# Optimization experiments

Measured on AMD Instinct MI355X. Metric: run time of the kernel, lower is better.

The kernel has to match this reference:

```python
import jax, jax.numpy as jnp
import numpy as np

N, D, H, G = 4096, 256, 4, 16
HEAD_DIM = D // H
LN_EPS = 1e-5
TEMP = 5.0


def setup_inputs() -> dict:
    key = jax.random.key(0)
    ks = jax.random.split(key, 12)
    s = 0.05  # weight init scale
    nrm = lambda k, shp: jax.random.normal(k, shp, jnp.float32) * s
    return {
        "x": jax.random.normal(ks[0], (N, D), jnp.float32),
        "Wq": nrm(ks[1], (D, D)), "bq": jnp.zeros((D,), jnp.float32),
        "Wk": nrm(ks[2], (D, D)), "bk": jnp.zeros((D,), jnp.float32),
        "Wv": nrm(ks[3], (D, D)), "bv": jnp.zeros((D,), jnp.float32),
        "Wv1": nrm(ks[4], (D, D // 2)), "bv1": jnp.zeros((D // 2,), jnp.float32),
        "Wv2": nrm(ks[5], (D // 2, 1)), "bv2": jnp.zeros((1,), jnp.float32),
        "Wc1": nrm(ks[6], (2 * D, D)), "bc1": jnp.zeros((D,), jnp.float32),
        "Wc2": nrm(ks[7], (D, 1)), "bc2": jnp.zeros((1,), jnp.float32),
        "gamma": jnp.ones((D,), jnp.float32),
        "beta": jnp.zeros((D,), jnp.float32),
        "batch": jnp.sort(jax.random.randint(ks[8], (N,), 0, G)),
    }


def reference(x, Wq, bq, Wk, bk, Wv, bv, Wv1, bv1, Wv2, bv2,
              Wc1, bc1, Wc2, bc2, gamma, beta, batch):
    n = x.shape[0]
    # multi-head projections -> [N, H, head_dim]
    Q = (x @ Wq + bq).reshape(n, H, HEAD_DIM)
    K = (x @ Wk + bk).reshape(n, H, HEAD_DIM)
    V = (x @ Wv + bv).reshape(n, H, HEAD_DIM)

    # dense scores [N, N, H], block-diagonal mask by graph membership
    scores = jnp.einsum('nhd,mhd->nmh', Q, K) / np.sqrt(HEAD_DIM).astype(np.float32)
    same_graph = (batch[:, None] == batch[None, :])  # [N, N]
    scores = jnp.where(same_graph[:, :, None], scores, -jnp.inf)
    probs = jax.nn.softmax(scores, axis=1)  # softmax over keys m (dim=1, as in torch)
    # dropout is identity in eval mode
    attended = jnp.einsum('nmh,mhd->nhd', probs, V).reshape(n, D)

    # vulnerability detector MLP: D -> D/2 -> 1, sigmoid
    vuln = jax.nn.sigmoid(jax.nn.relu(x @ Wv1 + bv1) @ Wv2 + bv2)[:, 0]

    # global max pool per graph, broadcast back to nodes
    graph_ctx = jax.ops.segment_max(x, batch, num_segments=G, indices_are_sorted=True)[batch]
    combined = jnp.concatenate([x, graph_ctx], axis=1)  # [N, 2D]
    ctx = jax.nn.sigmoid(jnp.tanh(combined @ Wc1 + bc1) @ Wc2 + bc2)[:, 0]

    mha_avg = probs.mean(axis=(1, 2))  # [N]
    w = 0.6 * vuln + 0.3 * ctx + 0.1 * mha_avg

    # per-graph segment softmax with temperature 5.0
    w5 = w * TEMP
    seg_max = jax.ops.segment_max(w5, batch, num_segments=G, indices_are_sorted=True)[batch]
    e = jnp.exp(w5 - seg_max)
    seg_sum = jax.ops.segment_sum(e, batch, num_segments=G, indices_are_sorted=True)[batch]
    att = e / seg_sum  # [N]

    out = attended * att[:, None] + x  # residual
    # LayerNorm over last dim
    mu = out.mean(axis=-1, keepdims=True)
    var = out.var(axis=-1, keepdims=True)
    out = (out - mu) * jax.lax.rsqrt(var + LN_EPS) * gamma + beta
    return out, att
```

## Files before the change

kernel.cpp:

```cpp
#include <hip/hip_runtime.h>
#include <math.h>

#define N_NODES 4096
#define DIM 256
#define NH 4
#define NG 16
#define LN_EPS 1e-5f
#define TEMP 5.0f
#define RSLACK 4160
#define PS_STRIDE 72
#define BS_STRIDE 264
#define QT_MAX 24
#define KC3 3
#define ATTN_BLOCKS (NG * QT_MAX * KC3)

typedef __attribute__((ext_vector_type(8))) short short8;
typedef __attribute__((ext_vector_type(4))) short short4_t;
typedef __attribute__((ext_vector_type(4))) float f32x4;

__device__ __forceinline__ unsigned short f2bf(float f) {
    unsigned u = __builtin_bit_cast(unsigned, f);
    u += 0x7FFFu + ((u >> 16) & 1u);
    return (unsigned short)(u >> 16);
}
__device__ __forceinline__ float bf2f(unsigned short u) {
    return __builtin_bit_cast(float, (unsigned)u << 16);
}
__device__ __forceinline__ float fsigmoid(float z) { return 1.f / (1.f + __expf(-z)); }
__device__ __forceinline__ float ftanh(float z) {
    float t = __expf(2.f * z);
    return (t - 1.f) / (t + 1.f);
}
__device__ __forceinline__ int seg_search(const int* __restrict__ batch, int g) {
    int lo = 0, hi = N_NODES;
    while (lo < hi) {
        int mid = (lo + hi) >> 1;
        if (batch[mid] < g) lo = mid + 1; else hi = mid;
    }
    return lo;
}

__device__ __forceinline__ short8 afrag_f32(const float* __restrict__ x, int row, int k0) {
    float4 a = *(const float4*)&x[(size_t)row * 256 + k0];
    float4 b = *(const float4*)&x[(size_t)row * 256 + k0 + 4];
    short8 r = {(short)f2bf(a.x), (short)f2bf(a.y), (short)f2bf(a.z), (short)f2bf(a.w),
                (short)f2bf(b.x), (short)f2bf(b.y), (short)f2bf(b.z), (short)f2bf(b.w)};
    return r;
}

__device__ __forceinline__ void ldsB(const float* __restrict__ W, int ws, int bn,
                                     unsigned short* __restrict__ Bs) {
    int c4 = (threadIdx.x & 15) * 4;
    int r0 = threadIdx.x >> 4;
    for (int p = 0; p < 16; ++p) {
        int k = p * 16 + r0;
        float4 wv = *(const float4*)&W[(size_t)k * ws + bn + c4];
        Bs[(c4 + 0) * BS_STRIDE + k] = f2bf(wv.x);
        Bs[(c4 + 1) * BS_STRIDE + k] = f2bf(wv.y);
        Bs[(c4 + 2) * BS_STRIDE + k] = f2bf(wv.z);
        Bs[(c4 + 3) * BS_STRIDE + k] = f2bf(wv.w);
    }
    __syncthreads();
}

__global__ __launch_bounds__(256) void k1_kernel(
    const float* __restrict__ x,
    const float* __restrict__ Wq, const float* __restrict__ bq,
    const float* __restrict__ Wk, const float* __restrict__ bk,
    const float* __restrict__ Wv, const float* __restrict__ bv,
    const float* __restrict__ Wv1, const float* __restrict__ bv1,
    const float* __restrict__ Wv2, const float* __restrict__ Wc1,
    const float* __restrict__ bc1, const int* __restrict__ batch,
    unsigned short* __restrict__ Qb, unsigned short* __restrict__ Kb,
    unsigned short* __restrict__ Vt, float* __restrict__ vacc2,
    float* __restrict__ Tpre, float* __restrict__ gcw, int* __restrict__ seg) {
    __shared__ __align__(16) char smem[64 * BS_STRIDE * 2];
    int id = blockIdx.x, tid = threadIdx.x;
    if (id < 16) {
        int g = id;
        int s = seg_search(batch, g), e = seg_search(batch, g + 1);
        float* red = (float*)smem;
        float* gl  = (float*)smem + 1024;
        int c4 = (tid & 63) * 4, way = tid >> 6;
        float4 mx = {-INFINITY, -INFINITY, -INFINITY, -INFINITY};
        for (int i = s + way; i < e; i += 4) {
            float4 v = *(const float4*)&x[(size_t)i * DIM + c4];
            mx.x = fmaxf(mx.x, v.x); mx.y = fmaxf(mx.y, v.y);
            mx.z = fmaxf(mx.z, v.z); mx.w = fmaxf(mx.w, v.w);
        }
        *(float4*)&red[way * 256 + c4] = mx;
        __syncthreads();
        if (way == 0) {
#pragma unroll
            for (int j = 0; j < 4; ++j) {
                float mm = fmaxf(fmaxf(red[c4 + j], red[256 + c4 + j]),
                                 fmaxf(red[512 + c4 + j], red[768 + c4 + j]));
                gl[c4 + j] = bf2f(f2bf(mm));
            }
        }
        __syncthreads();
        float a0 = 0.f, a1 = 0.f, a2 = 0.f, a3 = 0.f;
        for (int k = 0; k < 256; k += 4) {
            a0 += gl[k + 0] * Wc1[(size_t)(256 + k + 0) * 256 + tid];
            a1 += gl[k + 1] * Wc1[(size_t)(256 + k + 1) * 256 + tid];
            a2 += gl[k + 2] * Wc1[(size_t)(256 + k + 2) * 256 + tid];
            a3 += gl[k + 3] * Wc1[(size_t)(256 + k + 3) * 256 + tid];
        }
        gcw[g * 256 + tid] = (a0 + a1) + (a2 + a3);
        return;
    }
    if (id == 16) {
        if (tid <= NG) seg[tid] = seg_search(batch, tid);
        return;
    }
    int u = id - 17;
    unsigned short* Bs = (unsigned short*)smem;
    int w = tid >> 6, lane = tid & 63, m = lane & 15, quad = lane >> 4;
    if (u < 768) {
        int z = u >> 8, r = u & 255, bx = r & 63, by = r >> 6;
        const float* W = (z == 0) ? Wq : (z == 1) ? Wk : Wv;
        const float* bias = (z == 0) ? bq : (z == 1) ? bk : bv;
        ldsB(W, 256, by * 64, Bs);
        int rowA = bx * 64 + 16 * w + m;
        short8 a[8];
#pragma unroll
        for (int ks = 0; ks < 8; ++ks) a[ks] = afrag_f32(x, rowA, ks * 32 + quad * 8);
        int node0 = bx * 64 + 16 * w + quad * 4;
#pragma unroll
        for (int nt = 0; nt < 4; ++nt) {
            f32x4 acc = {0.f, 0.f, 0.f, 0.f};
#pragma unroll
            for (int ks = 0; ks < 8; ++ks) {
                short8 b = *(const short8*)&Bs[(nt * 16 + m) * BS_STRIDE + ks * 32 + quad * 8];
                acc = __builtin_amdgcn_mfma_f32_16x16x32_bf16(a[ks], b, acc, 0, 0, 0);
            }
            int col = by * 64 + nt * 16 + m;
            float bb = bias[col];
            if (z == 0) {
#pragma unroll
                for (int r2 = 0; r2 < 4; ++r2)
                    Qb[(size_t)(node0 + r2) * 256 + col] = f2bf((acc[r2] + bb) * 0.125f);
            } else if (z == 1) {
#pragma unroll
                for (int r2 = 0; r2 < 4; ++r2)
                    Kb[(size_t)(node0 + r2) * 256 + col] = f2bf(acc[r2] + bb);
            } else {
                short4_t pk = {(short)f2bf(acc[0] + bb), (short)f2bf(acc[1] + bb),
                               (short)f2bf(acc[2] + bb), (short)f2bf(acc[3] + bb)};
                *(short4_t*)&Vt[(size_t)col * RSLACK + node0] = pk;
            }
        }
    } else if (u < 896) {
        int r = u - 768, bx = r & 63, by = r >> 6;
        ldsB(Wv1, 128, by * 64, Bs);
        int rowA = bx * 64 + 16 * w + m;
        short8 a[8];
#pragma unroll
        for (int ks = 0; ks < 8; ++ks) a[ks] = afrag_f32(x, rowA, ks * 32 + quad * 8);
        int node0 = bx * 64 + 16 * w + quad * 4;
        float psum[4] = {0.f, 0.f, 0.f, 0.f};
#pragma unroll
        for (int nt = 0; nt < 4; ++nt) {
            f32x4 acc = {0.f, 0.f, 0.f, 0.f};
#pragma unroll
            for (int ks = 0; ks < 8; ++ks) {
                short8 b = *(const short8*)&Bs[(nt * 16 + m) * BS_STRIDE + ks * 32 + quad * 8];
                acc = __builtin_amdgcn_mfma_f32_16x16x32_bf16(a[ks], b, acc, 0, 0, 0);
            }
            int col = by * 64 + nt * 16 + m;
            float bb = bv1[col], wv = Wv2[col];
#pragma unroll
            for (int r2 = 0; r2 < 4; ++r2) psum[r2] += fmaxf(acc[r2] + bb, 0.f) * wv;
        }
#pragma unroll
        for (int r2 = 0; r2 < 4; ++r2) {
#pragma unroll
            for (int mm = 1; mm < 16; mm <<= 1) psum[r2] += __shfl_xor(psum[r2], mm);
            if (m == 0) vacc2[(size_t)(node0 + r2) * 2 + by] = psum[r2];
        }
    } else {
        int r = u - 896, bx = r & 63, by = r >> 6;
        ldsB(Wc1, 256, by * 64, Bs);
        int rowA = bx * 64 + 16 * w + m;
        short8 a[8];
#pragma unroll
        for (int ks = 0; ks < 8; ++ks) a[ks] = afrag_f32(x, rowA, ks * 32 + quad * 8);
        int node0 = bx * 64 + 16 * w + quad * 4;
#pragma unroll
        for (int nt = 0; nt < 4; ++nt) {
            f32x4 acc = {0.f, 0.f, 0.f, 0.f};
#pragma unroll
            for (int ks = 0; ks < 8; ++ks) {
                short8 b = *(const short8*)&Bs[(nt * 16 + m) * BS_STRIDE + ks * 32 + quad * 8];
                acc = __builtin_amdgcn_mfma_f32_16x16x32_bf16(a[ks], b, acc, 0, 0, 0);
            }
            int col = by * 64 + nt * 16 + m;
            float bb = bc1[col];
#pragma unroll
            for (int r2 = 0; r2 < 4; ++r2)
                Tpre[(size_t)(node0 + r2) * 256 + col] = acc[r2] + bb;
        }
    }
}

__global__ __launch_bounds__(256) void k2_kernel(
    const float* __restrict__ Tpre, const float* __restrict__ gcw,
    const float* __restrict__ Wc2, const int* __restrict__ batch,
    const unsigned short* __restrict__ Qb, const unsigned short* __restrict__ Kb,
    const unsigned short* __restrict__ Vt, const int* __restrict__ seg,
    unsigned short* __restrict__ Opart, float* __restrict__ Lpart,
    float* __restrict__ cacc) {
    __shared__ __align__(16) unsigned short Ps[4 * 16 * PS_STRIDE];
    int tid = threadIdx.x;
    if (blockIdx.x < 256) {
        int nl = tid >> 4, cs = (tid & 15) * 16;
        int node = blockIdx.x * 16 + nl;
        int g = batch[node];
        float sum = 0.f;
#pragma unroll
        for (int j = 0; j < 16; ++j) {
            int c = cs + j;
            sum += ftanh(Tpre[(size_t)node * 256 + c] + gcw[g * 256 + c]) * Wc2[c];
        }
#pragma unroll
        for (int mm = 1; mm < 16; mm <<= 1) sum += __shfl_xor(sum, mm);
        if ((tid & 15) == 0) cacc[node] = sum;
        return;
    }
    int w = tid >> 6, lane = tid & 63, m = lane & 15, quad = lane >> 4;
    int wid = (blockIdx.x - 256) * 4 + w;
    int g = wid / (KC3 * QT_MAX * NH);
    int r1 = wid - g * (KC3 * QT_MAX * NH);
    int kc = r1 / (QT_MAX * NH);
    int r2i = r1 - kc * (QT_MAX * NH);
    int qt = r2i >> 2, h = r2i & 3;
    int s = seg[g], e = seg[g + 1];
    int q0 = s + qt * 16;
    int kst = s + kc * 128;
    if (q0 >= e || kst >= e) return;
    int ken = min(e, kst + 128);

    short8 qa0 = *(const short8*)&Qb[(size_t)(q0 + m) * 256 + h * 64 + quad * 8];
    short8 qa1 = *(const short8*)&Qb[(size_t)(q0 + m) * 256 + h * 64 + 32 + quad * 8];
    short8 ones = {16256, 16256, 16256, 16256, 16256, 16256, 16256, 16256};
    f32x4 O[4];
    f32x4 Lacc = {0.f, 0.f, 0.f, 0.f};
#pragma unroll
    for (int nt = 0; nt < 4; ++nt) O[nt] = (f32x4){0.f, 0.f, 0.f, 0.f};
    int wbase = w * 16 * PS_STRIDE;

    for (int k0 = kst; k0 < ken; k0 += 64) {
        f32x4 S[4];
#pragma unroll
        for (int nt = 0; nt < 4; ++nt) {
            int key = k0 + nt * 16 + m;
            short8 kb0 = *(const short8*)&Kb[(size_t)key * 256 + h * 64 + quad * 8];
            short8 kb1 = *(const short8*)&Kb[(size_t)key * 256 + h * 64 + 32 + quad * 8];
            f32x4 sa = {0.f, 0.f, 0.f, 0.f};
            sa = __builtin_amdgcn_mfma_f32_16x16x32_bf16(qa0, kb0, sa, 0, 0, 0);
            sa = __builtin_amdgcn_mfma_f32_16x16x32_bf16(qa1, kb1, sa, 0, 0, 0);
            S[nt] = sa;
        }
        __builtin_amdgcn_wave_barrier();
#pragma unroll
        for (int nt = 0; nt < 4; ++nt) {
            bool valid = (k0 + nt * 16 + m) < e;
#pragma unroll
            for (int r3 = 0; r3 < 4; ++r3) {
                float p = valid ? __expf(S[nt][r3]) : 0.f;
                Ps[wbase + (quad * 4 + r3) * PS_STRIDE + nt * 16 + m] = f2bf(p);
            }
        }
        __builtin_amdgcn_wave_barrier();
        short8 pa0 = *(const short8*)&Ps[wbase + m * PS_STRIDE + quad * 8];
        short8 pa1 = *(const short8*)&Ps[wbase + m * PS_STRIDE + 32 + quad * 8];
        Lacc = __builtin_amdgcn_mfma_f32_16x16x32_bf16(pa0, ones, Lacc, 0, 0, 0);
        Lacc = __builtin_amdgcn_mfma_f32_16x16x32_bf16(pa1, ones, Lacc, 0, 0, 0);
#pragma unroll
        for (int nt = 0; nt < 4; ++nt) {
            const unsigned short* vrow = &Vt[(size_t)(h * 64 + nt * 16 + m) * RSLACK + k0];
            short8 vb0 = *(const short8*)&vrow[quad * 8];
            short8 vb1 = *(const short8*)&vrow[32 + quad * 8];
            O[nt] = __builtin_amdgcn_mfma_f32_16x16x32_bf16(pa0, vb0, O[nt], 0, 0, 0);
            O[nt] = __builtin_amdgcn_mfma_f32_16x16x32_bf16(pa1, vb1, O[nt], 0, 0, 0);
        }
    }
#pragma unroll
    for (int r3 = 0; r3 < 4; ++r3) {
        int q = q0 + quad * 4 + r3;
        if (q < e) {
            if (m == 0) Lpart[((size_t)kc * N_NODES + q) * 4 + h] = Lacc[r3];
#pragma unroll
            for (int nt = 0; nt < 4; ++nt)
                Opart[((size_t)kc * N_NODES + q) * 256 + h * 64 + nt * 16 + m] =
                    f2bf(O[nt][r3]);
        }
    }
}

__global__ __launch_bounds__(256) void k3_kernel(
    const unsigned short* __restrict__ Opart, const float* __restrict__ Lpart,
    const float* __restrict__ x, const float* __restrict__ vacc2,
    const float* __restrict__ cacc, const float* __restrict__ bv2,
    const float* __restrict__ bc2, const float* __restrict__ gamma,
    const float* __restrict__ beta, const int* __restrict__ batch,
    const int* __restrict__ seg, float* __restrict__ out,
    float* __restrict__ att_out) {
    __shared__ float wsc[776];
    __shared__ float gm[8], gsum[8];
    __shared__ float r1[4], r2[4];
    int tid = threadIdx.x;
    int n0 = blockIdx.x * 8;
    int gf = batch[n0], gl = batch[n0 + 7];
    int s0 = seg[gf], e1 = seg[gl + 1];
    float vb = bv2[0], cb = bc2[0];
    for (int j = s0 + tid; j < e1; j += 256) {
        float2 vv = *(const float2*)&vacc2[(size_t)j * 2];
        wsc[j - s0] = TEMP * (0.6f * fsigmoid(vv.x + vv.y + vb) +
                              0.3f * fsigmoid(cacc[j] + cb) + 0.1f / 4096.f);
    }
    __syncthreads();
    for (int g = gf; g <= gl; ++g) {
        int gs_ = seg[g], ge = seg[g + 1];
        float mx = -1e30f;
        for (int j = gs_ + tid; j < ge; j += 256) mx = fmaxf(mx, wsc[j - s0]);
#pragma unroll
        for (int k2 = 32; k2; k2 >>= 1) mx = fmaxf(mx, __shfl_xor(mx, k2));
        if ((tid & 63) == 0) r1[tid >> 6] = mx;
        __syncthreads();
        mx = fmaxf(fmaxf(r1[0], r1[1]), fmaxf(r1[2], r1[3]));
        float sm = 0.f;
        for (int j = gs_ + tid; j < ge; j += 256) sm += __expf(wsc[j - s0] - mx);
#pragma unroll
        for (int k2 = 32; k2; k2 >>= 1) sm += __shfl_xor(sm, k2);
        __syncthreads();
        if ((tid & 63) == 0) r2[tid >> 6] = sm;
        __syncthreads();
        if (tid == 0) {
            gm[g - gf] = mx;
            gsum[g - gf] = r2[0] + r2[1] + r2[2] + r2[3];
        }
        __syncthreads();
    }
    int h = tid >> 6;
    for (int i = 0; i < 8; ++i) {
        int n = n0 + i;
        int g = batch[n];
        int s = seg[g], e = seg[g + 1];
        float att_n = __expf(wsc[n - s0] - gm[g - gf]) / gsum[g - gf];
        if (tid == 0) att_out[n] = att_n;
        float L = 0.f, O = 0.f;
#pragma unroll
        for (int c = 0; c < KC3; ++c) {
            bool valid = (s + c * 128) < e;
            float lv = Lpart[((size_t)c * N_NODES + n) * 4 + h];
            float ov = bf2f(Opart[((size_t)c * N_NODES + n) * 256 + tid]);
            if (valid) { L += lv; O += ov; }
        }
        float o = (O / L) * att_n + x[(size_t)n * 256 + tid];
        float s1 = o, s2 = o * o;
#pragma unroll
        for (int k2 = 32; k2; k2 >>= 1) {
            s1 += __shfl_xor(s1, k2);
            s2 += __shfl_xor(s2, k2);
        }
        __syncthreads();
        if ((tid & 63) == 0) { r1[tid >> 6] = s1; r2[tid >> 6] = s2; }
        __syncthreads();
        float mu = (r1[0] + r1[1] + r1[2] + r1[3]) * (1.f / 256.f);
        float ms = (r2[0] + r2[1] + r2[2] + r2[3]) * (1.f / 256.f);
        float rs = rsqrtf(ms - mu * mu + LN_EPS);
        out[(size_t)n * 256 + tid] = (o - mu) * rs * gamma[tid] + beta[tid];
    }
}

extern "C" void kernel_launch(void* const* d_in, const int* in_sizes, int n_in,
                              void* d_out, int out_size, void* d_ws, size_t ws_size,
                              hipStream_t stream) {
    const float* x     = (const float*)d_in[0];
    const float* Wq    = (const float*)d_in[1];
    const float* bq    = (const float*)d_in[2];
    const float* Wk    = (const float*)d_in[3];
    const float* bk    = (const float*)d_in[4];
    const float* Wv    = (const float*)d_in[5];
    const float* bv    = (const float*)d_in[6];
    const float* Wv1   = (const float*)d_in[7];
    const float* bv1   = (const float*)d_in[8];
    const float* Wv2   = (const float*)d_in[9];
    const float* bv2   = (const float*)d_in[10];
    const float* Wc1   = (const float*)d_in[11];
    const float* bc1   = (const float*)d_in[12];
    const float* Wc2   = (const float*)d_in[13];
    const float* bc2   = (const float*)d_in[14];
    const float* gamma = (const float*)d_in[15];
    const float* beta  = (const float*)d_in[16];
    const int*   batch = (const int*)d_in[17];

    float* out = (float*)d_out;
    float* att = out + N_NODES * DIM;

    float* vacc2 = (float*)d_ws;
    float* cacc  = vacc2 + N_NODES * 2;
    float* gcw   = cacc + N_NODES;
    float* Lpart = gcw + NG * DIM;
    float* Tpre  = Lpart + KC3 * N_NODES * 4;
    int*   seg   = (int*)(Tpre + N_NODES * DIM);
    unsigned short* Qb    = (unsigned short*)(seg + 32);
    unsigned short* Kb    = Qb + RSLACK * DIM;
    unsigned short* Vt    = Kb + RSLACK * DIM;
    unsigned short* Opart = Vt + DIM * RSLACK;

    k1_kernel<<<1169, 256, 0, stream>>>(x, Wq, bq, Wk, bk, Wv, bv, Wv1, bv1, Wv2,
                                        Wc1, bc1, batch, Qb, Kb, Vt, vacc2, Tpre,
                                        gcw, seg);
    k2_kernel<<<256 + ATTN_BLOCKS, 256, 0, stream>>>(Tpre, gcw, Wc2, batch,
                                                     Qb, Kb, Vt, seg,
                                                     Opart, Lpart, cacc);
    k3_kernel<<<N_NODES / 8, 256, 0, stream>>>(Opart, Lpart, x, vacc2, cacc,
                                               bv2, bc2, gamma, beta, batch, seg,
                                               out, att);
}
```

Measured before the change: 169.0 us.

## Pre-convert x and weights to bf16 once; fuse ctx tanh epilogue into GEMM

Adds a prep kernel that converts x to bf16 and transposes and converts the Q/K/V/Wv1/Wc1 weights to bf16 once. It also computes the per-graph max-pool context and zeroes the ctx accumulator. The GEMM kernel then loads bf16 tiles directly, so it no longer re-converts fp32 in each of its many blocks. The Wc1 GEMM now applies tanh, the graph context and Wc2 in its epilogue and atomically accumulates ctx, which removes the Tpre round trip and the separate ctx pass in k2. The cost is an extra kernel launch and floating-point atomics, which make the ctx sum order nondeterministic.

```diff
diff --git a/kernel.cpp b/kernel.cpp
--- a/kernel.cpp
+++ b/kernel.cpp
@@ -40,47 +40,22 @@
     return lo;
 }
 
-__device__ __forceinline__ short8 afrag_f32(const float* __restrict__ x, int row, int k0) {
-    float4 a = *(const float4*)&x[(size_t)row * 256 + k0];
-    float4 b = *(const float4*)&x[(size_t)row * 256 + k0 + 4];
-    short8 r = {(short)f2bf(a.x), (short)f2bf(a.y), (short)f2bf(a.z), (short)f2bf(a.w),
-                (short)f2bf(b.x), (short)f2bf(b.y), (short)f2bf(b.z), (short)f2bf(b.w)};
-    return r;
-}
-
-__device__ __forceinline__ void ldsB(const float* __restrict__ W, int ws, int bn,
-                                     unsigned short* __restrict__ Bs) {
-    int c4 = (threadIdx.x & 15) * 4;
-    int r0 = threadIdx.x >> 4;
-    for (int p = 0; p < 16; ++p) {
-        int k = p * 16 + r0;
-        float4 wv = *(const float4*)&W[(size_t)k * ws + bn + c4];
-        Bs[(c4 + 0) * BS_STRIDE + k] = f2bf(wv.x);
-        Bs[(c4 + 1) * BS_STRIDE + k] = f2bf(wv.y);
-        Bs[(c4 + 2) * BS_STRIDE + k] = f2bf(wv.z);
-        Bs[(c4 + 3) * BS_STRIDE + k] = f2bf(wv.w);
-    }
-    __syncthreads();
-}
-
-__global__ __launch_bounds__(256) void k1_kernel(
-    const float* __restrict__ x,
-    const float* __restrict__ Wq, const float* __restrict__ bq,
-    const float* __restrict__ Wk, const float* __restrict__ bk,
-    const float* __restrict__ Wv, const float* __restrict__ bv,
-    const float* __restrict__ Wv1, const float* __restrict__ bv1,
-    const float* __restrict__ Wv2, const float* __restrict__ Wc1,
-    const float* __restrict__ bc1, const int* __restrict__ batch,
-    unsigned short* __restrict__ Qb, unsigned short* __restrict__ Kb,
-    unsigned short* __restrict__ Vt, float* __restrict__ vacc2,
-    float* __restrict__ Tpre, float* __restrict__ gcw, int* __restrict__ seg) {
-    __shared__ __align__(16) char smem[64 * BS_STRIDE * 2];
+__global__ __launch_bounds__(256) void k0_kernel(
+    const float* __restrict__ x, const float* __restrict__ Wq,
+    const float* __restrict__ Wk, const float* __restrict__ Wv,
+    const float* __restrict__ Wv1, const float* __restrict__ Wc1,
+    const int* __restrict__ batch,
+    unsigned short* __restrict__ xb, unsigned short* __restrict__ WqT,
+    unsigned short* __restrict__ WkT, unsigned short* __restrict__ WvT,
+    unsigned short* __restrict__ Wv1T, unsigned short* __restrict__ Wc1aT,
+    float* __restrict__ gcw, int* __restrict__ seg, float* __restrict__ cacc) {
+    __shared__ float sred[1280];
     int id = blockIdx.x, tid = threadIdx.x;
     if (id < 16) {
         int g = id;
         int s = seg_search(batch, g), e = seg_search(batch, g + 1);
-        float* red = (float*)smem;
-        float* gl  = (float*)smem + 1024;
+        float* red = sred;
+        float* gl  = sred + 1024;
         int c4 = (tid & 63) * 4, way = tid >> 6;
         float4 mx = {-INFINITY, -INFINITY, -INFINITY, -INFINITY};
         for (int i = s + way; i < e; i += 4) {
@@ -111,20 +86,81 @@
     }
     if (id == 16) {
         if (tid <= NG) seg[tid] = seg_search(batch, tid);
+        for (int i = tid; i < N_NODES; i += 256) cacc[i] = 0.f;
         return;
     }
-    int u = id - 17;
-    unsigned short* Bs = (unsigned short*)smem;
+    if (id < 81) {
+        int row = (id - 17) * 64 + (tid >> 2);
+        int c0 = (tid & 3) * 64;
+        const float* src = &x[(size_t)row * 256 + c0];
+        unsigned short* dst = &xb[(size_t)row * 256 + c0];
+#pragma unroll
+        for (int j = 0; j < 8; ++j) {
+            float4 a = *(const float4*)&src[j * 8];
+            float4 b = *(const float4*)&src[j * 8 + 4];
+            short8 r = {(short)f2bf(a.x), (short)f2bf(a.y), (short)f2bf(a.z), (short)f2bf(a.w),
+                        (short)f2bf(b.x), (short)f2bf(b.y), (short)f2bf(b.z), (short)f2bf(b.w)};
+            *(short8*)&dst[j * 8] = r;
+        }
+        return;
+    }
+    int t = id - 81;
+    const float* W; unsigned short* WT; int ncols, tt;
+    if (t < 16)      { W = Wq;  WT = WqT;   ncols = 256; tt = t; }
+    else if (t < 32) { W = Wk;  WT = WkT;   ncols = 256; tt = t - 16; }
+    else if (t < 48) { W = Wv;  WT = WvT;   ncols = 256; tt = t - 32; }
+    else if (t < 64) { W = Wc1; WT = Wc1aT; ncols = 256; tt = t - 48; }
+    else             { W = Wv1; WT = Wv1T;  ncols = 128; tt = t - 64; }
+    int c0 = (ncols == 256) ? (tt & 3) * 64 : (tt & 1) * 64;
+    int k0 = (ncols == 256) ? (tt >> 2) * 64 : (tt >> 1) * 64;
+    int col = c0 + (tid >> 2);
+    int kk0 = k0 + (tid & 3) * 16;
+    short8 r0v, r1v;
+#pragma unroll
+    for (int kk = 0; kk < 8; ++kk)
+        r0v[kk] = (short)f2bf(W[(size_t)(kk0 + kk) * ncols + col]);
+#pragma unroll
+    for (int kk = 0; kk < 8; ++kk)
+        r1v[kk] = (short)f2bf(W[(size_t)(kk0 + 8 + kk) * ncols + col]);
+    *(short8*)&WT[(size_t)col * 256 + kk0] = r0v;
+    *(short8*)&WT[(size_t)col * 256 + kk0 + 8] = r1v;
+}
+
+__device__ __forceinline__ void ldsB_bf(const unsigned short* __restrict__ WT, int bn,
+                                        unsigned short* __restrict__ Bs) {
+    const short8* src = (const short8*)&WT[(size_t)bn * 256 + threadIdx.x * 64];
+    unsigned short* dst = &Bs[(threadIdx.x >> 2) * BS_STRIDE + (threadIdx.x & 3) * 64];
+#pragma unroll
+    for (int j = 0; j < 8; ++j) *(short8*)&dst[j * 8] = src[j];
+    __syncthreads();
+}
+
+__global__ __launch_bounds__(256) void k1_kernel(
+    const unsigned short* __restrict__ xb,
+    const unsigned short* __restrict__ WqT, const unsigned short* __restrict__ WkT,
+    const unsigned short* __restrict__ WvT, const unsigned short* __restrict__ Wv1T,
+    const unsigned short* __restrict__ Wc1aT,
+    const float* __restrict__ bq, const float* __restrict__ bk,
+    const float* __restrict__ bv, const float* __restrict__ bv1,
+    const float* __restrict__ Wv2, const float* __restrict__ bc1,
+    const float* __restrict__ Wc2, const float* __restrict__ gcw,
+    const int* __restrict__ batch,
+    unsigned short* __restrict__ Qb, unsigned short* __restrict__ Kb,
+    unsigned short* __restrict__ Vt, float* __restrict__ vacc2,
+    float* __restrict__ cacc) {
+    __shared__ __align__(16) unsigned short Bs[64 * BS_STRIDE];
+    int u = blockIdx.x, tid = threadIdx.x;
     int w = tid >> 6, lane = tid & 63, m = lane & 15, quad = lane >> 4;
     if (u < 768) {
         int z = u >> 8, r = u & 255, bx = r & 63, by = r >> 6;
-        const float* W = (z == 0) ? Wq : (z == 1) ? Wk : Wv;
+        const unsigned short* WT = (z == 0) ? WqT : (z == 1) ? WkT : WvT;
         const float* bias = (z == 0) ? bq : (z == 1) ? bk : bv;
-        ldsB(W, 256, by * 64, Bs);
+        ldsB_bf(WT, by * 64, Bs);
         int rowA = bx * 64 + 16 * w + m;
         short8 a[8];
 #pragma unroll
-        for (int ks = 0; ks < 8; ++ks) a[ks] = afrag_f32(x, rowA, ks * 32 + quad * 8);
+        for (int ks = 0; ks < 8; ++ks)
+            a[ks] = *(const short8*)&xb[(size_t)rowA * 256 + ks * 32 + quad * 8];
         int node0 = bx * 64 + 16 * w + quad * 4;
 #pragma unroll
         for (int nt = 0; nt < 4; ++nt) {
@@ -152,11 +188,12 @@
         }
     } else if (u < 896) {
         int r = u - 768, bx = r & 63, by = r >> 6;
-        ldsB(Wv1, 128, by * 64, Bs);
+        ldsB_bf(Wv1T, by * 64, Bs);
         int rowA = bx * 64 + 16 * w + m;
         short8 a[8];
 #pragma unroll
-        for (int ks = 0; ks < 8; ++ks) a[ks] = afrag_f32(x, rowA, ks * 32 + quad * 8);
+        for (int ks = 0; ks < 8; ++ks)
+            a[ks] = *(const short8*)&xb[(size_t)rowA * 256 + ks * 32 + quad * 8];
         int node0 = bx * 64 + 16 * w + quad * 4;
         float psum[4] = {0.f, 0.f, 0.f, 0.f};
 #pragma unroll
@@ -180,12 +217,16 @@
         }
     } else {
         int r = u - 896, bx = r & 63, by = r >> 6;
-        ldsB(Wc1, 256, by * 64, Bs);
+        ldsB_bf(Wc1aT, by * 64, Bs);
         int rowA = bx * 64 + 16 * w + m;
         short8 a[8];
 #pragma unroll
-        for (int ks = 0; ks < 8; ++ks) a[ks] = afrag_f32(x, rowA, ks * 32 + quad * 8);
+        for (int ks = 0; ks < 8; ++ks)
+            a[ks] = *(const short8*)&xb[(size_t)rowA * 256 + ks * 32 + quad * 8];
         int node0 = bx * 64 + 16 * w + quad * 4;
+        int g0 = batch[node0], g1 = batch[node0 + 1];
+        int g2 = batch[node0 + 2], g3 = batch[node0 + 3];
+        float psum[4] = {0.f, 0.f, 0.f, 0.f};
 #pragma unroll
         for (int nt = 0; nt < 4; ++nt) {
             f32x4 acc = {0.f, 0.f, 0.f, 0.f};
@@ -195,40 +236,30 @@
                 acc = __builtin_amdgcn_mfma_f32_16x16x32_bf16(a[ks], b, acc, 0, 0, 0);
             }
             int col = by * 64 + nt * 16 + m;
-            float bb = bc1[col];
-#pragma unroll
-            for (int r2 = 0; r2 < 4; ++r2)
-                Tpre[(size_t)(node0 + r2) * 256 + col] = acc[r2] + bb;
+            float bb = bc1[col], wc = Wc2[col];
+            const float* gc = &gcw[col];
+            psum[0] += ftanh(acc[0] + bb + gc[g0 * 256]) * wc;
+            psum[1] += ftanh(acc[1] + bb + gc[g1 * 256]) * wc;
+            psum[2] += ftanh(acc[2] + bb + gc[g2 * 256]) * wc;
+            psum[3] += ftanh(acc[3] + bb + gc[g3 * 256]) * wc;
+        }
+#pragma unroll
+        for (int r2 = 0; r2 < 4; ++r2) {
+#pragma unroll
+            for (int mm = 1; mm < 16; mm <<= 1) psum[r2] += __shfl_xor(psum[r2], mm);
+            if (m == 0) atomicAdd(&cacc[node0 + r2], psum[r2]);
         }
     }
 }
 
 __global__ __launch_bounds__(256) void k2_kernel(
-    const float* __restrict__ Tpre, const float* __restrict__ gcw,
-    const float* __restrict__ Wc2, const int* __restrict__ batch,
     const unsigned short* __restrict__ Qb, const unsigned short* __restrict__ Kb,
     const unsigned short* __restrict__ Vt, const int* __restrict__ seg,
-    unsigned short* __restrict__ Opart, float* __restrict__ Lpart,
-    float* __restrict__ cacc) {
+    unsigned short* __restrict__ Opart, float* __restrict__ Lpart) {
     __shared__ __align__(16) unsigned short Ps[4 * 16 * PS_STRIDE];
     int tid = threadIdx.x;
-    if (blockIdx.x < 256) {
-        int nl = tid >> 4, cs = (tid & 15) * 16;
-        int node = blockIdx.x * 16 + nl;
-        int g = batch[node];
-        float sum = 0.f;
-#pragma unroll
-        for (int j = 0; j < 16; ++j) {
-            int c = cs + j;
-            sum += ftanh(Tpre[(size_t)node * 256 + c] + gcw[g * 256 + c]) * Wc2[c];
-        }
-#pragma unroll
-        for (int mm = 1; mm < 16; mm <<= 1) sum += __shfl_xor(sum, mm);
-        if ((tid & 15) == 0) cacc[node] = sum;
-        return;
-    }
     int w = tid >> 6, lane = tid & 63, m = lane & 15, quad = lane >> 4;
-    int wid = (blockIdx.x - 256) * 4 + w;
+    int wid = blockIdx.x * 4 + w;
     int g = wid / (KC3 * QT_MAX * NH);
     int r1 = wid - g * (KC3 * QT_MAX * NH);
     int kc = r1 / (QT_MAX * NH);
@@ -403,19 +434,25 @@
     float* cacc  = vacc2 + N_NODES * 2;
     float* gcw   = cacc + N_NODES;
     float* Lpart = gcw + NG * DIM;
-    float* Tpre  = Lpart + KC3 * N_NODES * 4;
-    int*   seg   = (int*)(Tpre + N_NODES * DIM);
-    unsigned short* Qb    = (unsigned short*)(seg + 32);
+    int*   seg   = (int*)(Lpart + KC3 * N_NODES * 4);
+    unsigned short* xb    = (unsigned short*)(seg + 32);
+    unsigned short* WqT   = xb + N_NODES * DIM;
+    unsigned short* WkT   = WqT + DIM * DIM;
+    unsigned short* WvT   = WkT + DIM * DIM;
+    unsigned short* Wc1aT = WvT + DIM * DIM;
+    unsigned short* Wv1T  = Wc1aT + DIM * DIM;
+    unsigned short* Qb    = Wv1T + (DIM / 2) * DIM;
     unsigned short* Kb    = Qb + RSLACK * DIM;
     unsigned short* Vt    = Kb + RSLACK * DIM;
     unsigned short* Opart = Vt + DIM * RSLACK;
 
-    k1_kernel<<<1169, 256, 0, stream>>>(x, Wq, bq, Wk, bk, Wv, bv, Wv1, bv1, Wv2,
-                                        Wc1, bc1, batch, Qb, Kb, Vt, vacc2, Tpre,
-                                        gcw, seg);
-    k2_kernel<<<256 + ATTN_BLOCKS, 256, 0, stream>>>(Tpre, gcw, Wc2, batch,
-                                                     Qb, Kb, Vt, seg,
-                                                     Opart, Lpart, cacc);
+    k0_kernel<<<153, 256, 0, stream>>>(x, Wq, Wk, Wv, Wv1, Wc1, batch,
+                                       xb, WqT, WkT, WvT, Wv1T, Wc1aT,
+                                       gcw, seg, cacc);
+    k1_kernel<<<1152, 256, 0, stream>>>(xb, WqT, WkT, WvT, Wv1T, Wc1aT,
+                                        bq, bk, bv, bv1, Wv2, bc1, Wc2, gcw, batch,
+                                        Qb, Kb, Vt, vacc2, cacc);
+    k2_kernel<<<ATTN_BLOCKS, 256, 0, stream>>>(Qb, Kb, Vt, seg, Opart, Lpart);
     k3_kernel<<<N_NODES / 8, 256, 0, stream>>>(Opart, Lpart, x, vacc2, cacc,
                                                bv2, bc2, gamma, beta, batch, seg,
                                                out, att);
```

Measured after the change: 175.1 us. 3.6% more time.

## Drop key-chunk split in attention, prefetch V fragments, unroll gcw loads

Applied to the files above, without the earlier changes.

Each attention wave now covers the whole key range of its graph instead of one of three 128-key chunks. This removes the partial-result writes and the three-way merge in the final kernel, and the attention blocks are ordered before the context-MLP blocks. V fragments are loaded right after the QK MFMAs, ahead of the softmax, to hide load latency. The graph-context GEMV batches 32 weight loads per step, and the segment max loop is unrolled. The cost is fewer waves with longer serial loops, which lowers parallelism for large graphs.

```diff
diff --git a/kernel.cpp b/kernel.cpp
--- a/kernel.cpp
+++ b/kernel.cpp
@@ -11,8 +11,7 @@
 #define PS_STRIDE 72
 #define BS_STRIDE 264
 #define QT_MAX 24
-#define KC3 3
-#define ATTN_BLOCKS (NG * QT_MAX * KC3)
+#define K2_ATTN_BLOCKS (NG * QT_MAX)
 
 typedef __attribute__((ext_vector_type(8))) short short8;
 typedef __attribute__((ext_vector_type(4))) short short4_t;
@@ -83,6 +82,7 @@
         float* gl  = (float*)smem + 1024;
         int c4 = (tid & 63) * 4, way = tid >> 6;
         float4 mx = {-INFINITY, -INFINITY, -INFINITY, -INFINITY};
+#pragma unroll 8
         for (int i = s + way; i < e; i += 4) {
             float4 v = *(const float4*)&x[(size_t)i * DIM + c4];
             mx.x = fmaxf(mx.x, v.x); mx.y = fmaxf(mx.y, v.y);
@@ -99,14 +99,16 @@
             }
         }
         __syncthreads();
-        float a0 = 0.f, a1 = 0.f, a2 = 0.f, a3 = 0.f;
-        for (int k = 0; k < 256; k += 4) {
-            a0 += gl[k + 0] * Wc1[(size_t)(256 + k + 0) * 256 + tid];
-            a1 += gl[k + 1] * Wc1[(size_t)(256 + k + 1) * 256 + tid];
-            a2 += gl[k + 2] * Wc1[(size_t)(256 + k + 2) * 256 + tid];
-            a3 += gl[k + 3] * Wc1[(size_t)(256 + k + 3) * 256 + tid];
-        }
-        gcw[g * 256 + tid] = (a0 + a1) + (a2 + a3);
+        float ac[4] = {0.f, 0.f, 0.f, 0.f};
+        for (int kb = 0; kb < 256; kb += 32) {
+            float v[32];
+#pragma unroll
+            for (int j = 0; j < 32; ++j)
+                v[j] = Wc1[(size_t)(256 + kb + j) * 256 + tid];
+#pragma unroll
+            for (int j = 0; j < 32; ++j) ac[j & 3] += gl[kb + j] * v[j];
+        }
+        gcw[g * 256 + tid] = (ac[0] + ac[1]) + (ac[2] + ac[3]);
         return;
     }
     if (id == 16) {
@@ -212,9 +214,10 @@
     float* __restrict__ cacc) {
     __shared__ __align__(16) unsigned short Ps[4 * 16 * PS_STRIDE];
     int tid = threadIdx.x;
-    if (blockIdx.x < 256) {
+    if (blockIdx.x >= K2_ATTN_BLOCKS) {
+        int id2 = blockIdx.x - K2_ATTN_BLOCKS;
         int nl = tid >> 4, cs = (tid & 15) * 16;
-        int node = blockIdx.x * 16 + nl;
+        int node = id2 * 16 + nl;
         int g = batch[node];
         float sum = 0.f;
 #pragma unroll
@@ -228,17 +231,13 @@
         return;
     }
     int w = tid >> 6, lane = tid & 63, m = lane & 15, quad = lane >> 4;
-    int wid = (blockIdx.x - 256) * 4 + w;
-    int g = wid / (KC3 * QT_MAX * NH);
-    int r1 = wid - g * (KC3 * QT_MAX * NH);
-    int kc = r1 / (QT_MAX * NH);
-    int r2i = r1 - kc * (QT_MAX * NH);
+    int wid = blockIdx.x * 4 + w;
+    int g = wid / (QT_MAX * NH);
+    int r2i = wid - g * (QT_MAX * NH);
     int qt = r2i >> 2, h = r2i & 3;
     int s = seg[g], e = seg[g + 1];
     int q0 = s + qt * 16;
-    int kst = s + kc * 128;
-    if (q0 >= e || kst >= e) return;
-    int ken = min(e, kst + 128);
+    if (q0 >= e) return;
 
     short8 qa0 = *(const short8*)&Qb[(size_t)(q0 + m) * 256 + h * 64 + quad * 8];
     short8 qa1 = *(const short8*)&Qb[(size_t)(q0 + m) * 256 + h * 64 + 32 + quad * 8];
@@ -249,7 +248,7 @@
     for (int nt = 0; nt < 4; ++nt) O[nt] = (f32x4){0.f, 0.f, 0.f, 0.f};
     int wbase = w * 16 * PS_STRIDE;
 
-    for (int k0 = kst; k0 < ken; k0 += 64) {
+    for (int k0 = s; k0 < e; k0 += 64) {
         f32x4 S[4];
 #pragma unroll
         for (int nt = 0; nt < 4; ++nt) {
@@ -261,6 +260,13 @@
             sa = __builtin_amdgcn_mfma_f32_16x16x32_bf16(qa1, kb1, sa, 0, 0, 0);
             S[nt] = sa;
         }
+        short8 vb[4][2];
+#pragma unroll
+        for (int nt = 0; nt < 4; ++nt) {
+            const unsigned short* vrow = &Vt[(size_t)(h * 64 + nt * 16 + m) * RSLACK + k0];
+            vb[nt][0] = *(const short8*)&vrow[quad * 8];
+            vb[nt][1] = *(const short8*)&vrow[32 + quad * 8];
+        }
         __builtin_amdgcn_wave_barrier();
 #pragma unroll
         for (int nt = 0; nt < 4; ++nt) {
@@ -278,22 +284,18 @@
         Lacc = __builtin_amdgcn_mfma_f32_16x16x32_bf16(pa1, ones, Lacc, 0, 0, 0);
 #pragma unroll
         for (int nt = 0; nt < 4; ++nt) {
-            const unsigned short* vrow = &Vt[(size_t)(h * 64 + nt * 16 + m) * RSLACK + k0];
-            short8 vb0 = *(const short8*)&vrow[quad * 8];
-            short8 vb1 = *(const short8*)&vrow[32 + quad * 8];
-            O[nt] = __builtin_amdgcn_mfma_f32_16x16x32_bf16(pa0, vb0, O[nt], 0, 0, 0);
-            O[nt] = __builtin_amdgcn_mfma_f32_16x16x32_bf16(pa1, vb1, O[nt], 0, 0, 0);
+            O[nt] = __builtin_amdgcn_mfma_f32_16x16x32_bf16(pa0, vb[nt][0], O[nt], 0, 0, 0);
+            O[nt] = __builtin_amdgcn_mfma_f32_16x16x32_bf16(pa1, vb[nt][1], O[nt], 0, 0, 0);
         }
     }
 #pragma unroll
     for (int r3 = 0; r3 < 4; ++r3) {
         int q = q0 + quad * 4 + r3;
         if (q < e) {
-            if (m == 0) Lpart[((size_t)kc * N_NODES + q) * 4 + h] = Lacc[r3];
+            if (m == 0) Lpart[(size_t)q * 4 + h] = Lacc[r3];
 #pragma unroll
             for (int nt = 0; nt < 4; ++nt)
-                Opart[((size_t)kc * N_NODES + q) * 256 + h * 64 + nt * 16 + m] =
-                    f2bf(O[nt][r3]);
+                Opart[(size_t)q * 256 + h * 64 + nt * 16 + m] = f2bf(O[nt][r3]);
         }
     }
 }
@@ -346,17 +348,10 @@
     for (int i = 0; i < 8; ++i) {
         int n = n0 + i;
         int g = batch[n];
-        int s = seg[g], e = seg[g + 1];
         float att_n = __expf(wsc[n - s0] - gm[g - gf]) / gsum[g - gf];
         if (tid == 0) att_out[n] = att_n;
-        float L = 0.f, O = 0.f;
-#pragma unroll
-        for (int c = 0; c < KC3; ++c) {
-            bool valid = (s + c * 128) < e;
-            float lv = Lpart[((size_t)c * N_NODES + n) * 4 + h];
-            float ov = bf2f(Opart[((size_t)c * N_NODES + n) * 256 + tid]);
-            if (valid) { L += lv; O += ov; }
-        }
+        float L = Lpart[(size_t)n * 4 + h];
+        float O = bf2f(Opart[(size_t)n * 256 + tid]);
         float o = (O / L) * att_n + x[(size_t)n * 256 + tid];
         float s1 = o, s2 = o * o;
 #pragma unroll
@@ -403,7 +398,7 @@
     float* cacc  = vacc2 + N_NODES * 2;
     float* gcw   = cacc + N_NODES;
     float* Lpart = gcw + NG * DIM;
-    float* Tpre  = Lpart + KC3 * N_NODES * 4;
+    float* Tpre  = Lpart + N_NODES * 4;
     int*   seg   = (int*)(Tpre + N_NODES * DIM);
     unsigned short* Qb    = (unsigned short*)(seg + 32);
     unsigned short* Kb    = Qb + RSLACK * DIM;
@@ -413,9 +408,9 @@
     k1_kernel<<<1169, 256, 0, stream>>>(x, Wq, bq, Wk, bk, Wv, bv, Wv1, bv1, Wv2,
                                         Wc1, bc1, batch, Qb, Kb, Vt, vacc2, Tpre,
                                         gcw, seg);
-    k2_kernel<<<256 + ATTN_BLOCKS, 256, 0, stream>>>(Tpre, gcw, Wc2, batch,
-                                                     Qb, Kb, Vt, seg,
-                                                     Opart, Lpart, cacc);
+    k2_kernel<<<K2_ATTN_BLOCKS + 256, 256, 0, stream>>>(Tpre, gcw, Wc2, batch,
+                                                        Qb, Kb, Vt, seg,
+                                                        Opart, Lpart, cacc);
     k3_kernel<<<N_NODES / 8, 256, 0, stream>>>(Opart, Lpart, x, vacc2, cacc,
                                                bv2, bc2, gamma, beta, batch, seg,
                                                out, att);
```

New measurement: 167.1 us. No clear change (-1.2%).
